# Optimization experiments

Hardware: AMD Instinct MI355X
Metric: run time of the kernel (lower is better)

The kernel has to match this reference:

```python
import jax, jax.numpy as jnp
import numpy as np

DIM = 192; RES = (8, 56, 56); HEADS = 6; WS = (2, 7, 7); SS = (1, 3, 3)
B = 2
N_WIN_TOK = WS[0] * WS[1] * WS[2]  # 98


def _rel_pos_index():
    # 3D Swin relative position index, (N, N) int
    Wd, Wh, Ww = WS
    coords = np.stack(np.meshgrid(np.arange(Wd), np.arange(Wh), np.arange(Ww), indexing='ij'))
    coords = coords.reshape(3, -1)  # (3, N)
    rel = (coords[:, :, None] - coords[:, None, :]).transpose(1, 2, 0)  # (N, N, 3)
    rel[:, :, 0] += Wd - 1
    rel[:, :, 1] += Wh - 1
    rel[:, :, 2] += Ww - 1
    rel[:, :, 0] *= (2 * Wh - 1) * (2 * Ww - 1)
    rel[:, :, 1] *= (2 * Ww - 1)
    return rel.sum(-1)


def _attn_mask():
    # shifted-window mask (nW, N, N), 0 / -100
    D, H, W = RES; Wd, Wh, Ww = WS; sd, sh, sw = SS
    img = np.zeros((D, H, W))
    cnt = 0
    for ds in (slice(0, -Wd), slice(-Wd, -sd), slice(-sd, None)):
        for hs in (slice(0, -Wh), slice(-Wh, -sh), slice(-sh, None)):
            for ws_ in (slice(0, -Ww), slice(-Ww, -sw), slice(-sw, None)):
                img[ds, hs, ws_] = cnt
                cnt += 1
    win = img.reshape(D // Wd, Wd, H // Wh, Wh, W // Ww, Ww)
    win = win.transpose(0, 2, 4, 1, 3, 5).reshape(-1, N_WIN_TOK)  # (nW, N)
    diff = win[:, :, None] - win[:, None, :]
    return np.where(diff != 0, -100.0, 0.0).astype(np.float32)


_REL_IDX = _rel_pos_index()
_MASK = _attn_mask()


def _window_partition(x):
    # (B, D, H, W, C) -> (B*nW, N, C)
    Bb, D, H, W, C = x.shape
    Wd, Wh, Ww = WS
    x = x.reshape(Bb, D // Wd, Wd, H // Wh, Wh, W // Ww, Ww, C)
    x = x.transpose(0, 1, 3, 5, 2, 4, 6, 7)
    return x.reshape(-1, N_WIN_TOK, C)


def _window_reverse(x, Bb):
    # (B*nW, N, C) -> (B, D, H, W, C)
    D, H, W = RES; Wd, Wh, Ww = WS
    C = x.shape[-1]
    x = x.reshape(Bb, D // Wd, H // Wh, W // Ww, Wd, Wh, Ww, C)
    x = x.transpose(0, 1, 4, 2, 5, 3, 6, 7)
    return x.reshape(Bb, D, H, W, C)


def _layernorm(x, g, b, eps=1e-5):
    mu = jnp.mean(x, -1, keepdims=True)
    var = jnp.var(x, -1, keepdims=True)
    return (x - mu) * jax.lax.rsqrt(var + eps) * g + b


def setup_inputs() -> dict:
    key = jax.random.key(0)
    ks = jax.random.split(key, 8)
    L = RES[0] * RES[1] * RES[2]
    s = 0.02
    return {
        'x': jax.random.normal(ks[0], (B, L, DIM), jnp.float32),
        'norm1_g': jnp.ones((DIM,), jnp.float32),
        'norm1_b': jnp.zeros((DIM,), jnp.float32),
        'qkv_w': jax.random.normal(ks[1], (3 * DIM, DIM), jnp.float32) * s,
        'qkv_b': jax.random.normal(ks[2], (3 * DIM,), jnp.float32) * s,
        'rel_table': jax.random.normal(ks[3], ((2 * WS[0] - 1) * (2 * WS[1] - 1) * (2 * WS[2] - 1), HEADS), jnp.float32) * s,
        'norm2_g': jnp.ones((DIM,), jnp.float32),
        'norm2_b': jnp.zeros((DIM,), jnp.float32),
        'mlp_w1': jax.random.normal(ks[4], (4 * DIM, DIM), jnp.float32) * s,
        'mlp_b1': jax.random.normal(ks[5], (4 * DIM,), jnp.float32) * s,
        'mlp_w2': jax.random.normal(ks[6], (DIM, 4 * DIM), jnp.float32) * s,
        'mlp_b2': jax.random.normal(ks[7], (4 * DIM // 4,), jnp.float32) * s,
    }


def reference(x, norm1_g, norm1_b, qkv_w, qkv_b, rel_table, norm2_g, norm2_b, mlp_w1, mlp_b1, mlp_w2, mlp_b2):
    Bb, L, C = x.shape
    D, H, W = RES
    hd = C // HEADS
    scale = hd ** (-0.5)

    short_cut = x
    xn = _layernorm(x, norm1_g, norm1_b).reshape(Bb, D, H, W, C)
    xs = jnp.roll(xn, (-SS[0], -SS[1], -SS[2]), axis=(1, 2, 3))
    xw = _window_partition(xs)  # (Bn, N, C)
    Bn, N, _ = xw.shape

    # qkv grouping matches original: (nH hD qkv), qkv fastest axis
    qkv = (jnp.einsum('bnc,oc->bno', xw, qkv_w) + qkv_b).reshape(Bn, N, HEADS, hd, 3)
    q = qkv[..., 0].transpose(0, 2, 1, 3)  # (Bn, nH, N, hd)
    k = qkv[..., 1].transpose(0, 2, 1, 3)
    v = qkv[..., 2].transpose(0, 2, 1, 3)

    attn = jnp.einsum('bhnd,bhmd->bhnm', q, k) * scale
    bias = rel_table[jnp.asarray(_REL_IDX.reshape(-1))].reshape(N, N, HEADS)
    attn = attn + bias.transpose(2, 0, 1)[None]  # (Bn, nH, N, N)

    mask = jnp.asarray(_MASK)  # (nW, N, N)
    nW = mask.shape[0]
    attn = attn.reshape(Bb, nW, HEADS, N, N) + mask[None, :, None]
    attn = jax.nn.softmax(attn.reshape(Bn, HEADS, N, N), axis=-1)

    out = jnp.einsum('bhnm,bhmd->bhnd', attn, v)
    out = out.transpose(0, 2, 1, 3).reshape(Bn, N, C)

    xr = _window_reverse(out, Bb)
    x2 = jnp.roll(xr, (SS[0], SS[1], SS[2]), axis=(1, 2, 3)).reshape(Bb, L, C) + short_cut

    short_cut2 = x2
    h = _layernorm(x2, norm2_g, norm2_b)
    h = jax.nn.relu(jnp.einsum('blc,oc->blo', h, mlp_w1) + mlp_b1)
    h = jax.nn.relu(jnp.einsum('blo,co->blc', h, mlp_w2) + mlp_b2)
    return h + short_cut2
```

## Files before the change

### kernel.cpp

```cpp
#include <hip/hip_runtime.h>

typedef unsigned short u16;
typedef unsigned int   u32;
typedef __attribute__((ext_vector_type(4))) float f32x4;
typedef __attribute__((ext_vector_type(8))) short s16x8;
typedef __attribute__((ext_vector_type(4))) u32   u32x4;
typedef __attribute__((ext_vector_type(4))) u16   u16x4;

#define DEV static __device__ __forceinline__

DEV float bf2f(u16 a) { union { u32 u; float f; } x; x.u = ((u32)a) << 16; return x.f; }
DEV u16 f2bf(float f) {
  union { float f; u32 u; } x; x.f = f;
  u32 r = (x.u + 0x7FFFu + ((x.u >> 16) & 1u)) >> 16;
  return (u16)r;
}
DEV float wsum(float v) {
#pragma unroll
  for (int m = 32; m; m >>= 1) v += __shfl_xor(v, m, 64);
  return v;
}

DEV int xcd_swz(int bid, int nwg) {
  int q = nwg >> 3, r = nwg & 7;
  int xcd = bid & 7, idx = bid >> 3;
  return (xcd < r ? xcd * (q + 1) : r * (q + 1) + (xcd - r) * q) + idx;
}

DEV void gload16(const void* g, void* l) {
  __builtin_amdgcn_global_load_lds(
      (const __attribute__((address_space(1))) u32*)g,
      (__attribute__((address_space(3))) u32*)l, 16, 0, 0);
}

DEV const s16x8* frag(const u16* lds, int row, int s) {
  int sw = (s & ~7) | ((s & 7) ^ (row & 7));
  return reinterpret_cast<const s16x8*>(
      reinterpret_cast<const char*>(lds) + row * 384 + sw * 16);
}


__global__ __launch_bounds__(256) void k_prep(
    const float* __restrict__ qkvw, const float* __restrict__ qkvb,
    u16* __restrict__ qkvwb, float* __restrict__ pbias,
    const float* __restrict__ w1, u16* __restrict__ w1b,
    const float* __restrict__ relt, u16* __restrict__ biasT,
    const float* __restrict__ x, const float* __restrict__ n1g,
    const float* __restrict__ n1b, u16* __restrict__ xw)
{
  int b = blockIdx.x, tid = threadIdx.x;
  if (b < 108) {
    const float sc = 0.17677669529663687f;
    int i = b * 256 + tid;
    if (i < 27648) {
      int np = i / 48, c = i - np * 48;
      int t = np / 192, rem = np - t * 192;
      int head = rem >> 5, dd = rem & 31;
      int o = head * 96 + dd * 3 + t;
      float s2 = (t == 0) ? sc : 1.f;
      f32x4 v = reinterpret_cast<const f32x4*>(qkvw)[o * 48 + c];
      u16x4 ov; ov[0] = f2bf(v[0] * s2); ov[1] = f2bf(v[1] * s2);
      ov[2] = f2bf(v[2] * s2); ov[3] = f2bf(v[3] * s2);
      reinterpret_cast<u16x4*>(qkvwb)[i] = ov;
    }
    if (i < 576) {
      int t = i / 192, rem = i - t * 192;
      int head = rem >> 5, dd = rem & 31;
      pbias[i] = qkvb[head * 96 + dd * 3 + t] * ((t == 0) ? sc : 1.f);
    }
  } else if (b < 252) {
    int i = (b - 108) * 256 + tid;
    if (i < 36864) {
      f32x4 v = reinterpret_cast<const f32x4*>(w1)[i];
      u16x4 o; o[0] = f2bf(v[0]); o[1] = f2bf(v[1]); o[2] = f2bf(v[2]); o[3] = f2bf(v[3]);
      reinterpret_cast<u16x4*>(w1b)[i] = o;
    }
  } else if (b < 2604) {
    int i = (b - 252) * 256 + tid;
    if (i >= 602112) return;
    int t = i % 112; int rem = i / 112;
    int j = rem % 112; rem /= 112;
    int h = rem % 6; int c = rem / 6;
    if (j >= 98) { biasT[i] = f2bf(-1e30f); return; }
    if (t >= 98) { biasT[i] = 0; return; }
    int td = t >= 49, tr = t - td * 49, th = tr / 7, tw = tr - th * 7;
    int jd = j >= 49, jr = j - jd * 49, jh = jr / 7, jw = jr - jh * 7;
    int lin_t = td * 169 + th * 13 + tw;
    int lin_j = jd * 169 + jh * 13 + jw;
    float bias = relt[(lin_t - lin_j + 253) * 6 + h];
    int cd = (c >> 2) & 1, ch = (c >> 1) & 1, cw = c & 1;
    int cnt_t = (cd ? (1 + td) : 0) * 9 + (ch ? (1 + (th >= 4)) : 0) * 3 + (cw ? (1 + (tw >= 4)) : 0);
    int cnt_j = (cd ? (1 + jd) : 0) * 9 + (ch ? (1 + (jh >= 4)) : 0) * 3 + (cw ? (1 + (jw >= 4)) : 0);
    if (cnt_t != cnt_j) bias -= 100.f;
    biasT[i] = f2bf(bias);
  } else {
    int row  = (b - 2604) * 4 + (tid >> 6);
    int lane = tid & 63;
    int win = row / 98, tok = row - win * 98;
    int bb = win >> 8, wrem = win & 255;
    int wd = wrem >> 6, wh = (wrem >> 3) & 7, ww = wrem & 7;
    int td = tok >= 49; int tr = tok - td * 49; int th = tr / 7, tw = tr - th * 7;
    int dsrc = (wd * 2 + td + 1) & 7;
    int hs = wh * 7 + th + 3; if (hs >= 56) hs -= 56;
    int wsc = ww * 7 + tw + 3; if (wsc >= 56) wsc -= 56;
    const float* xr = x + ((size_t)bb * 25088 + (size_t)dsrc * 3136 + hs * 56 + wsc) * 192;
    float v0 = xr[lane], v1 = xr[lane + 64], v2 = xr[lane + 128];
    float mu  = wsum(v0 + v1 + v2) * (1.f / 192.f);
    float sq  = wsum(v0 * v0 + v1 * v1 + v2 * v2) * (1.f / 192.f);
    float inv = rsqrtf(sq - mu * mu + 1e-5f);
    u16* orow = xw + (size_t)row * 192;
    orow[lane      ] = f2bf((v0 - mu) * inv * n1g[lane      ] + n1b[lane      ]);
    orow[lane + 64 ] = f2bf((v1 - mu) * inv * n1g[lane + 64 ] + n1b[lane + 64 ]);
    orow[lane + 128] = f2bf((v2 - mu) * inv * n1g[lane + 128] + n1b[lane + 128]);
  }
}

__global__ __launch_bounds__(256) void k_merge_ln2(
    const float* __restrict__ x, const u16* __restrict__ ao,
    const float* __restrict__ g, const float* __restrict__ b,
    u16* __restrict__ x2b, u16* __restrict__ xn2)
{
  int m = blockIdx.x * 4 + (threadIdx.x >> 6);
  int lane = threadIdx.x & 63;
  int bb = m / 25088, l = m - bb * 25088;
  int d = l / 3136; int rem = l - d * 3136; int h = rem / 56, w = rem - h * 56;
  int dsh = (d + 7) & 7;
  int hsh = h - 3; if (hsh < 0) hsh += 56;
  int wsh = w - 3; if (wsh < 0) wsh += 56;
  int wd = dsh >> 1, td = dsh & 1;
  int wh = hsh / 7, th = hsh - wh * 7;
  int ww = wsh / 7, tw = wsh - ww * 7;
  int win = (bb << 8) + (wd << 6) + (wh << 3) + ww;
  int tok = td * 49 + th * 7 + tw;
  const u16* ar = ao + ((size_t)win * 98 + tok) * 192;
  const float* xr = x + (size_t)m * 192;
  float v0 = xr[lane      ] + bf2f(ar[lane      ]);
  float v1 = xr[lane + 64 ] + bf2f(ar[lane + 64 ]);
  float v2 = xr[lane + 128] + bf2f(ar[lane + 128]);
  u16* x2r = x2b + (size_t)m * 192;
  x2r[lane] = f2bf(v0); x2r[lane + 64] = f2bf(v1); x2r[lane + 128] = f2bf(v2);
  float mu  = wsum(v0 + v1 + v2) * (1.f / 192.f);
  float sq  = wsum(v0 * v0 + v1 * v1 + v2 * v2) * (1.f / 192.f);
  float inv = rsqrtf(sq - mu * mu + 1e-5f);
  u16* nr = xn2 + (size_t)m * 192;
  nr[lane      ] = f2bf((v0 - mu) * inv * g[lane      ] + b[lane      ]);
  nr[lane + 64 ] = f2bf((v1 - mu) * inv * g[lane + 64 ] + b[lane + 64 ]);
  nr[lane + 128] = f2bf((v2 - mu) * inv * g[lane + 128] + b[lane + 128]);
}

template<bool RELU, int NTOT>
__global__ __launch_bounds__(256) void k_gemm3(
    const u16* __restrict__ A, const u16* __restrict__ Wb, const float* __restrict__ bias,
    u16* __restrict__ C, const float* __restrict__ w2src, u16* __restrict__ w2dst)
{
  constexpr int MG = 8;
  constexpr int NB = NTOT / 96;
  constexpr int MAINW = NB * 98;
  __shared__ u16 As[2][64 * 192];
  int bid = blockIdx.x;
  if (RELU && bid >= MAINW) {
    int i = (bid - MAINW) * 256 + threadIdx.x;
    if (i < 36864) {
      f32x4 v = reinterpret_cast<const f32x4*>(w2src)[i];
      u16x4 o; o[0] = f2bf(v[0]); o[1] = f2bf(v[1]); o[2] = f2bf(v[2]); o[3] = f2bf(v[3]);
      reinterpret_cast<u16x4*>(w2dst)[i] = o;
    }
    return;
  }
  bid = xcd_swz(bid, MAINW);
  int mg = bid / NB, nb = bid - mg * NB;
  int n0 = nb * 96;
  int m_base = mg * (MG * 64);
  int tid = threadIdx.x, lane = tid & 63, wv = tid >> 6;
  int lr = lane & 15, lg = lane >> 4;
  int wm = wv >> 1, wn = wv & 1;

  auto stage = [&](int buf, int mt) {
    const char* gb = (const char*)(A + (size_t)(m_base + mt * 64) * 192);
    char* lb = (char*)As[buf] + wv * 6144;
#pragma unroll
    for (int c = 0; c < 6144; c += 1024) {
      int o = wv * 6144 + c + lane * 16;
      int row = (int)((u32)o / 384u);
      int slot = (o - row * 384) >> 4;
      int sw = (slot & ~7) | ((slot & 7) ^ (row & 7));
      gload16(gb + (size_t)row * 384 + sw * 16, lb + c);
    }
  };

  stage(0, 0);

  s16x8 wf[3][6];
  const u16* wbase = Wb + (size_t)(n0 + wn * 48 + lr) * 192 + lg * 8;
#pragma unroll
  for (int nf = 0; nf < 3; ++nf)
#pragma unroll
    for (int ks = 0; ks < 6; ++ks)
      wf[nf][ks] = *reinterpret_cast<const s16x8*>(wbase + (size_t)nf * 16 * 192 + ks * 32);
  float bs[3];
#pragma unroll
  for (int nf = 0; nf < 3; ++nf) bs[nf] = bias[n0 + wn * 48 + nf * 16 + lr];

  __syncthreads();
  for (int i = 0; i < MG; ++i) {
    int cur = i & 1;
    if (i + 1 < MG) stage(cur ^ 1, i + 1);
    f32x4 acc[2][3];
#pragma unroll
    for (int a = 0; a < 2; ++a)
#pragma unroll
      for (int nf = 0; nf < 3; ++nf) acc[a][nf] = {0.f, 0.f, 0.f, 0.f};
#pragma unroll
    for (int ks = 0; ks < 6; ++ks) {
      int s = ks * 4 + lg;
      s16x8 a0 = *frag(As[cur], wm * 32 + lr, s);
      s16x8 a1 = *frag(As[cur], wm * 32 + 16 + lr, s);
#pragma unroll
      for (int nf = 0; nf < 3; ++nf) {
        acc[0][nf] = __builtin_amdgcn_mfma_f32_16x16x32_bf16(a0, wf[nf][ks], acc[0][nf], 0, 0, 0);
        acc[1][nf] = __builtin_amdgcn_mfma_f32_16x16x32_bf16(a1, wf[nf][ks], acc[1][nf], 0, 0, 0);
      }
    }
    int m0 = m_base + i * 64;
#pragma unroll
    for (int mi = 0; mi < 2; ++mi)
#pragma unroll
      for (int nf = 0; nf < 3; ++nf)
#pragma unroll
        for (int r = 0; r < 4; ++r) {
          int m = m0 + wm * 32 + mi * 16 + lg * 4 + r;
          int n = n0 + wn * 48 + nf * 16 + lr;
          float val = acc[mi][nf][r] + bs[nf];
          if (RELU) val = fmaxf(val, 0.f);
          C[(size_t)m * NTOT + n] = f2bf(val);
        }
    __syncthreads();
  }
}

__global__ __launch_bounds__(512) void k_gemm2mlp2(
    const u16* __restrict__ A, const u16* __restrict__ Wb, const float* __restrict__ bias,
    const u16* __restrict__ x2b, float* __restrict__ of)
{
  constexpr int MB = 784;
  constexpr int KTOT = 768;
  __shared__ u16 As[64 * 192];
  __shared__ u16 Ws[96 * 192];
  int bid = xcd_swz(blockIdx.x, 2 * MB);
  int mb = bid >> 1, nb = bid & 1;
  int m0 = mb * 64, n0 = nb * 96;
  int tid = threadIdx.x, lane = tid & 63, wv = tid >> 6;
  int lr = lane & 15, lg = lane >> 4;
  int wm = wv >> 1, wn = wv & 1;

  f32x4 acc[3];
#pragma unroll
  for (int j = 0; j < 3; ++j) acc[j] = {0.f, 0.f, 0.f, 0.f};

  for (int kc = 0; kc < 4; ++kc) {
    if (kc) __syncthreads();
    if (wv < 4) {
      const char* gb = (const char*)(A + (size_t)m0 * KTOT + kc * 192);
      int base = wv * 6144;
#pragma unroll
      for (int c = 0; c < 6144; c += 1024) {
        int o = base + c + lane * 16;
        int row = (int)((u32)o / 384u);
        int slot = (o - row * 384) >> 4;
        int sw = (slot & ~7) | ((slot & 7) ^ (row & 7));
        gload16(gb + (size_t)row * (KTOT * 2) + sw * 16, (char*)As + base + c);
      }
    } else {
      const char* gb = (const char*)(Wb + (size_t)n0 * KTOT + kc * 192);
      int base = (wv - 4) * 9216;
#pragma unroll
      for (int c = 0; c < 9216; c += 1024) {
        int o = base + c + lane * 16;
        int row = (int)((u32)o / 384u);
        int slot = (o - row * 384) >> 4;
        int sw = (slot & ~7) | ((slot & 7) ^ (row & 7));
        gload16(gb + (size_t)row * (KTOT * 2) + sw * 16, (char*)Ws + base + c);
      }
    }
    __syncthreads();
#pragma unroll
    for (int ks = 0; ks < 6; ++ks) {
      int s = ks * 4 + lg;
      s16x8 a0 = *frag(As, wm * 16 + lr, s);
#pragma unroll
      for (int nf = 0; nf < 3; ++nf) {
        s16x8 bfr = *frag(Ws, wn * 48 + nf * 16 + lr, s);
        acc[nf] = __builtin_amdgcn_mfma_f32_16x16x32_bf16(a0, bfr, acc[nf], 0, 0, 0);
      }
    }
  }
#pragma unroll
  for (int nf = 0; nf < 3; ++nf)
#pragma unroll
    for (int r = 0; r < 4; ++r) {
      int m = m0 + wm * 16 + lg * 4 + r;
      int n = n0 + wn * 48 + nf * 16 + lr;
      size_t idx = (size_t)m * 192 + n;
      of[idx] = fmaxf(acc[nf][r] + bias[n], 0.f) + bf2f(x2b[idx]);
    }
}

__global__ __launch_bounds__(448, 2) void k_attn_mfma(
    const u16* __restrict__ qkvc, const u16* __restrict__ biasT, u16* __restrict__ ao)
{
  __shared__ u16 P[7][16 * 128];
  __shared__ u16 Vt[32 * 136];
  __shared__ u16 Ks[98 * 40];

  int bid = xcd_swz(blockIdx.x, 3072);
  int win = bid / 6, head = bid - win * 6;
  int tid = threadIdx.x, lane = tid & 63, wv = tid >> 6;
  int lr = lane & 15, lg = lane >> 4;
  size_t rb = (size_t)(win * 98) * 576;
  const u16* qp0 = qkvc + rb + head * 32;
  const u16* kp0 = qkvc + rb + 192 + head * 32;
  const u16* vp0 = qkvc + rb + 384 + head * 32;

  int wrem = win & 255;
  int wd = wrem >> 6, wh = (wrem >> 3) & 7, ww = wrem & 7;
  int cls = ((wd == 3) ? 4 : 0) | ((wh == 7) ? 2 : 0) | ((ww == 7) ? 1 : 0);
  const u16* bT = biasT + (size_t)(cls * 6 + head) * 112 * 112;

  int qrow = wv * 16 + lr; if (qrow > 97) qrow = 97;
  s16x8 qf = *reinterpret_cast<const s16x8*>(qp0 + (size_t)qrow * 576 + lg * 8);
  u16x4 b4[7];
#pragma unroll
  for (int j = 0; j < 7; ++j) {
    int col = j * 16 + lr;
    b4[j] = *reinterpret_cast<const u16x4*>(bT + (size_t)col * 112 + wv * 16 + lg * 4);
  }

  for (int u = tid; u < 98 * 16; u += 448) {
    int tok = u >> 4, dp = (u & 15) * 2;
    u32 w = *reinterpret_cast<const u32*>(vp0 + (size_t)tok * 576 + dp);
    Vt[dp * 136 + tok]       = (u16)(w & 0xFFFFu);
    Vt[(dp + 1) * 136 + tok] = (u16)(w >> 16);
    u32 wk = *reinterpret_cast<const u32*>(kp0 + (size_t)tok * 576 + dp);
    *reinterpret_cast<u32*>(&Ks[tok * 40 + dp]) = wk;
  }
  for (int u = tid; u < 32 * 19; u += 448) {
    int d = u / 19, kslot = u - d * 19;
    *reinterpret_cast<u32*>(reinterpret_cast<char*>(Vt) + d * 272 + 196 + kslot * 4) = 0;
  }
  __syncthreads();

  f32x4 s[7];
  __builtin_amdgcn_s_setprio(1);
#pragma unroll
  for (int j = 0; j < 7; ++j) {
    int row = j * 16 + lr; if (row > 97) row = 97;
    s16x8 kfj = *reinterpret_cast<const s16x8*>(&Ks[row * 40 + lg * 8]);
    f32x4 c4;
#pragma unroll
    for (int r = 0; r < 4; ++r) c4[r] = bf2f(b4[j][r]);
    s[j] = __builtin_amdgcn_mfma_f32_16x16x32_bf16(qf, kfj, c4, 0, 0, 0);
  }
  __builtin_amdgcn_s_setprio(0);

  float sm[4] = {0.f, 0.f, 0.f, 0.f};
#pragma unroll
  for (int j = 0; j < 7; ++j)
#pragma unroll
    for (int r = 0; r < 4; ++r) {
      float p = __expf(s[j][r]);
      s[j][r] = p;
      sm[r] += p;
    }
#pragma unroll
  for (int m = 1; m < 16; m <<= 1)
#pragma unroll
    for (int r = 0; r < 4; ++r) sm[r] += __shfl_xor(sm[r], m, 64);
  float rinv[4];
#pragma unroll
  for (int r = 0; r < 4; ++r) rinv[r] = 1.f / sm[r];

#pragma unroll
  for (int j = 0; j < 7; ++j) {
    int col = j * 16 + lr;
    int slot = col >> 3, wi = col & 7;
#pragma unroll
    for (int r = 0; r < 4; ++r) {
      int lrow = lg * 4 + r;
      P[wv][lrow * 128 + (((slot ^ (lrow & 7)) << 3) | wi)] = f2bf(s[j][r]);
    }
  }
  if (lane < 32) {
    int lrow = lr;
    int slot = 14 + lg;
    u32x4 z4 = {0u, 0u, 0u, 0u};
    *reinterpret_cast<u32x4*>(&P[wv][lrow * 128 + ((slot ^ (lrow & 7)) << 3)]) = z4;
  }

  f32x4 o0 = {0.f, 0.f, 0.f, 0.f}, o1 = {0.f, 0.f, 0.f, 0.f};
  __builtin_amdgcn_s_setprio(1);
#pragma unroll
  for (int kc = 0; kc < 4; ++kc) {
    int slot = kc * 4 + lg;
    s16x8 pf = *reinterpret_cast<const s16x8*>(&P[wv][lr * 128 + ((slot ^ (lr & 7)) << 3)]);
    s16x8 vf0 = *reinterpret_cast<const s16x8*>(&Vt[lr * 136 + kc * 32 + lg * 8]);
    s16x8 vf1 = *reinterpret_cast<const s16x8*>(&Vt[(16 + lr) * 136 + kc * 32 + lg * 8]);
    o0 = __builtin_amdgcn_mfma_f32_16x16x32_bf16(pf, vf0, o0, 0, 0, 0);
    o1 = __builtin_amdgcn_mfma_f32_16x16x32_bf16(pf, vf1, o1, 0, 0, 0);
  }
  __builtin_amdgcn_s_setprio(0);
#pragma unroll
  for (int r = 0; r < 4; ++r) {
    int t = wv * 16 + lg * 4 + r;
    if (t < 98) {
      size_t ob = ((size_t)win * 98 + t) * 192 + head * 32;
      ao[ob + lr]      = f2bf(o0[r] * rinv[r]);
      ao[ob + 16 + lr] = f2bf(o1[r] * rinv[r]);
    }
  }
}

extern "C" void kernel_launch(void* const* d_in, const int* in_sizes, int n_in,
                              void* d_out, int out_size, void* d_ws, size_t ws_size,
                              hipStream_t stream) {
  (void)in_sizes; (void)n_in; (void)out_size; (void)ws_size;
  const float* x    = (const float*)d_in[0];
  const float* n1g  = (const float*)d_in[1];
  const float* n1b  = (const float*)d_in[2];
  const float* qkvw = (const float*)d_in[3];
  const float* qkvb = (const float*)d_in[4];
  const float* relt = (const float*)d_in[5];
  const float* n2g  = (const float*)d_in[6];
  const float* n2b  = (const float*)d_in[7];
  const float* w1   = (const float*)d_in[8];
  const float* b1   = (const float*)d_in[9];
  const float* w2   = (const float*)d_in[10];
  const float* b2   = (const float*)d_in[11];
  float* out = (float*)d_out;
  char* ws = (char*)d_ws;

  constexpr size_t SZB = 50176ull * 192 * 2;
  u16*  xw    = (u16*)(ws);
  u16*  qkvc  = (u16*)(ws + SZB);
  u16*  x2b   = (u16*)(ws + SZB);
  u16*  xn2   = (u16*)(ws + 3 * SZB);
  u16*  h1    = (u16*)(ws + 4 * SZB);
  u16*  ao    = xw;
  u16*  w2b   = xw;

  u16*   qkvwb = (u16*)out;
  u16*   w1b   = (u16*)((char*)out + 221184);
  float* pbias = (float*)((char*)out + 516096);
  u16*   biasT = (u16*)((char*)out + 520192);

  k_prep<<<2604 + 12544, 256, 0, stream>>>(qkvw, qkvb, qkvwb, pbias, w1, w1b, relt, biasT,
                                           x, n1g, n1b, xw);
  k_gemm3<false, 576><<<6 * 98, 256, 0, stream>>>(xw, qkvwb, pbias, qkvc, nullptr, nullptr);
  k_attn_mfma<<<3072, 448, 0, stream>>>(qkvc, biasT, ao);
  k_merge_ln2<<<12544, 256, 0, stream>>>(x, ao, n2g, n2b, x2b, xn2);
  k_gemm3<true, 768><<<8 * 98 + 144, 256, 0, stream>>>(xn2, w1b, b1, h1, w2, w2b);
  k_gemm2mlp2<<<784 * 2, 512, 0, stream>>>(h1, w2b, b2, x2b, out);
}
```

Before: 149.4 us.

## Restructure MLP2 GEMM: full-N tiles, register-resident weights, double-buffered A

The second MLP GEMM now uses one 256-thread block per 64-row tile covering all 192 output columns, instead of two 512-thread blocks split along N. Weight fragments are loaded straight from global memory into registers per wave rather than staged through LDS. The activation tile is double-buffered in LDS so the next K chunk loads while the current one is computed. Each A tile is read from global once, and each wave does more MFMAs per LDS fragment, which raises register pressure and halves the block count.

```diff
diff --git a/kernel.cpp b/kernel.cpp
--- a/kernel.cpp
+++ b/kernel.cpp
@@ -238,71 +238,75 @@
   }
 }
 
-__global__ __launch_bounds__(512) void k_gemm2mlp2(
+__global__ __launch_bounds__(256) void k_mlp2(
     const u16* __restrict__ A, const u16* __restrict__ Wb, const float* __restrict__ bias,
     const u16* __restrict__ x2b, float* __restrict__ of)
 {
-  constexpr int MB = 784;
-  constexpr int KTOT = 768;
-  __shared__ u16 As[64 * 192];
-  __shared__ u16 Ws[96 * 192];
-  int bid = xcd_swz(blockIdx.x, 2 * MB);
-  int mb = bid >> 1, nb = bid & 1;
-  int m0 = mb * 64, n0 = nb * 96;
+  __shared__ u16 As[2][64 * 192];
+  int bid = xcd_swz(blockIdx.x, 784);
+  int m0 = bid * 64;
   int tid = threadIdx.x, lane = tid & 63, wv = tid >> 6;
   int lr = lane & 15, lg = lane >> 4;
-  int wm = wv >> 1, wn = wv & 1;
-
-  f32x4 acc[3];
-#pragma unroll
-  for (int j = 0; j < 3; ++j) acc[j] = {0.f, 0.f, 0.f, 0.f};
-
+  int n0 = wv * 48;
+
+  auto stage = [&](int buf, int kc) {
+    const char* gb = (const char*)(A + (size_t)m0 * 768 + kc * 192);
+    char* lb = (char*)As[buf] + wv * 6144;
+#pragma unroll
+    for (int c = 0; c < 6144; c += 1024) {
+      int o = wv * 6144 + c + lane * 16;
+      int row = (int)((u32)o / 384u);
+      int slot = (o - row * 384) >> 4;
+      int sw = (slot & ~7) | ((slot & 7) ^ (row & 7));
+      gload16(gb + (size_t)row * 1536 + sw * 16, lb + c);
+    }
+  };
+
+  f32x4 acc[4][3];
+#pragma unroll
+  for (int mi = 0; mi < 4; ++mi)
+#pragma unroll
+    for (int nf = 0; nf < 3; ++nf) acc[mi][nf] = {0.f, 0.f, 0.f, 0.f};
+  float bs[3];
+#pragma unroll
+  for (int nf = 0; nf < 3; ++nf) bs[nf] = bias[n0 + nf * 16 + lr];
+
+  stage(0, 0);
+  __syncthreads();
   for (int kc = 0; kc < 4; ++kc) {
-    if (kc) __syncthreads();
-    if (wv < 4) {
-      const char* gb = (const char*)(A + (size_t)m0 * KTOT + kc * 192);
-      int base = wv * 6144;
-#pragma unroll
-      for (int c = 0; c < 6144; c += 1024) {
-        int o = base + c + lane * 16;
-        int row = (int)((u32)o / 384u);
-        int slot = (o - row * 384) >> 4;
-        int sw = (slot & ~7) | ((slot & 7) ^ (row & 7));
-        gload16(gb + (size_t)row * (KTOT * 2) + sw * 16, (char*)As + base + c);
-      }
-    } else {
-      const char* gb = (const char*)(Wb + (size_t)n0 * KTOT + kc * 192);
-      int base = (wv - 4) * 9216;
-#pragma unroll
-      for (int c = 0; c < 9216; c += 1024) {
-        int o = base + c + lane * 16;
-        int row = (int)((u32)o / 384u);
-        int slot = (o - row * 384) >> 4;
-        int sw = (slot & ~7) | ((slot & 7) ^ (row & 7));
-        gload16(gb + (size_t)row * (KTOT * 2) + sw * 16, (char*)Ws + base + c);
-      }
-    }
-    __syncthreads();
+    int cur = kc & 1;
+    if (kc < 3) stage(cur ^ 1, kc + 1);
+    s16x8 wf[3][6];
+    const u16* wbase = Wb + (size_t)(n0 + lr) * 768 + kc * 192 + lg * 8;
+#pragma unroll
+    for (int nf = 0; nf < 3; ++nf)
+#pragma unroll
+      for (int ks = 0; ks < 6; ++ks)
+        wf[nf][ks] = *reinterpret_cast<const s16x8*>(wbase + (size_t)nf * 16 * 768 + ks * 32);
 #pragma unroll
     for (int ks = 0; ks < 6; ++ks) {
       int s = ks * 4 + lg;
-      s16x8 a0 = *frag(As, wm * 16 + lr, s);
-#pragma unroll
-      for (int nf = 0; nf < 3; ++nf) {
-        s16x8 bfr = *frag(Ws, wn * 48 + nf * 16 + lr, s);
-        acc[nf] = __builtin_amdgcn_mfma_f32_16x16x32_bf16(a0, bfr, acc[nf], 0, 0, 0);
+#pragma unroll
+      for (int mi = 0; mi < 4; ++mi) {
+        s16x8 a0 = *frag(As[cur], mi * 16 + lr, s);
+#pragma unroll
+        for (int nf = 0; nf < 3; ++nf)
+          acc[mi][nf] = __builtin_amdgcn_mfma_f32_16x16x32_bf16(a0, wf[nf][ks], acc[mi][nf], 0, 0, 0);
       }
     }
-  }
-#pragma unroll
-  for (int nf = 0; nf < 3; ++nf)
-#pragma unroll
-    for (int r = 0; r < 4; ++r) {
-      int m = m0 + wm * 16 + lg * 4 + r;
-      int n = n0 + wn * 48 + nf * 16 + lr;
-      size_t idx = (size_t)m * 192 + n;
-      of[idx] = fmaxf(acc[nf][r] + bias[n], 0.f) + bf2f(x2b[idx]);
-    }
+    __syncthreads();
+  }
+#pragma unroll
+  for (int mi = 0; mi < 4; ++mi)
+#pragma unroll
+    for (int nf = 0; nf < 3; ++nf)
+#pragma unroll
+      for (int r = 0; r < 4; ++r) {
+        int m = m0 + mi * 16 + lg * 4 + r;
+        int n = n0 + nf * 16 + lr;
+        size_t idx = (size_t)m * 192 + n;
+        of[idx] = fmaxf(acc[mi][nf][r] + bs[nf], 0.f) + bf2f(x2b[idx]);
+      }
 }
 
 __global__ __launch_bounds__(448, 2) void k_attn_mfma(
@@ -458,5 +462,5 @@
   k_attn_mfma<<<3072, 448, 0, stream>>>(qkvc, biasT, ao);
   k_merge_ln2<<<12544, 256, 0, stream>>>(x, ao, n2g, n2b, x2b, xn2);
   k_gemm3<true, 768><<<8 * 98 + 144, 256, 0, stream>>>(xn2, w1b, b1, h1, w2, w2b);
-  k_gemm2mlp2<<<784 * 2, 512, 0, stream>>>(h1, w2b, b2, x2b, out);
-}
+  k_mlp2<<<784, 256, 0, stream>>>(h1, w2b, b2, x2b, out);
+}
```

Result: slower. 167.3 us (+11.9%).
